# Optimization experiments

Hardware: AMD Instinct MI355X
Metric: run time of the kernel (lower is better)

Reference implementation:

```python
import jax, jax.numpy as jnp
import numpy as np

B, S, E, H = 2, 2048, 512, 8
MLP = 4 * E


def _ln(x, w, b, eps=1e-5):
    m = jnp.mean(x, -1, keepdims=True)
    v = jnp.var(x, -1, keepdims=True)
    return (x - m) / jnp.sqrt(v + eps) * w + b


def setup_inputs() -> dict:
    key = jax.random.key(0)
    ks = jax.random.split(key, 8)
    s = lambda k, shape: (jax.random.normal(k, shape, jnp.float32) * 0.02)
    return {
        "query": jax.random.normal(ks[0], (B, S, E), jnp.float32),
        "attn_gate": jax.random.uniform(ks[1], (B * H, S, S), jnp.float32),
        "in_proj_w": s(ks[2], (3 * E, E)),
        "in_proj_b": jnp.zeros((3 * E,), jnp.float32),
        "out_w": s(ks[3], (E, E)),
        "out_b": jnp.zeros((E,), jnp.float32),
        "ln1_w": jnp.ones((E,), jnp.float32),
        "ln1_b": jnp.zeros((E,), jnp.float32),
        "ln2_w": jnp.ones((E,), jnp.float32),
        "ln2_b": jnp.zeros((E,), jnp.float32),
        "w1": s(ks[4], (MLP, E)),
        "b1": jnp.zeros((MLP,), jnp.float32),
        "w2": s(ks[5], (E, MLP)),
        "b2": jnp.zeros((E,), jnp.float32),
    }


def reference(query, attn_gate, in_proj_w, in_proj_b, out_w, out_b,
              ln1_w, ln1_b, ln2_w, ln2_b, w1, b1, w2, b2):
    b, s, e = query.shape
    h = H
    dh = e // h
    nq = _ln(query, ln1_w, ln1_b)  # pre-LN; key=value=normed query (self-attn)
    Wq, Wk, Wv = jnp.split(in_proj_w, 3, axis=0)
    bq, bk, bv = jnp.split(in_proj_b, 3, axis=0)
    q = nq @ Wq.T + bq
    k = nq @ Wk.T + bk
    v = nq @ Wv.T + bv
    # faithful raw reshape (B,S,E)->(B*H,S,Dh), as in the torch .view
    q = q.reshape(b * h, s, dh)
    k = k.reshape(b * h, s, dh)
    v = v.reshape(b * h, s, dh)
    w = jnp.einsum("bqd,bkd->bqk", q, k)  # no 1/sqrt(d) scaling in source
    w = w * attn_gate
    w = w / (jnp.sum(w, -1, keepdims=True) + 1e-12)  # sum-renormalization
    w = jax.nn.softmax(w, axis=-1)
    o = jnp.einsum("bqk,bkd->bqd", w, v)  # (B*H, S, Dh)
    o = jnp.swapaxes(o, 0, 1).reshape(s, b, e)  # faithful transpose+view
    o = o @ out_w.T + out_b
    o = jnp.swapaxes(o, 0, 1)  # back to batch_first (B,S,E)
    x = query + o
    hmid = _ln(x, ln2_w, ln2_b)
    x = x + (jax.nn.gelu(hmid @ w1.T + b1, approximate=False) @ w2.T + b2)
    attn_weights = w.reshape(b, h, s, s).mean(axis=1)  # average_attn_weights=True
    return (x, attn_weights)
```

## Files before the change

kernel.cpp:

```cpp
#include <hip/hip_runtime.h>
#include <cstdint>
#include <cstddef>

typedef __bf16 bf16_t;
typedef __bf16 bf16x8 __attribute__((ext_vector_type(8)));
typedef float  f32x4  __attribute__((ext_vector_type(4)));

#define S_LEN   2048
#define E_DIM   512
#define H_NUM   8
#define DH      64
#define MLP_DIM 2048

static __device__ __forceinline__ unsigned short f2bfu(float f){
  bf16_t h = (bf16_t)f;
  return __builtin_bit_cast(unsigned short, h);
}

static __device__ __forceinline__ float gelu_f(float v){
  return 0.5f*v*(1.0f + erff(v*0.70710678118654752f));
}

__global__ __launch_bounds__(256) void cvt_kernel(const float* __restrict__ s,
                                                  bf16_t* __restrict__ d, int n){
  int i = (blockIdx.x*256 + threadIdx.x)*4;
  if (i < n){
    float4 v = *(const float4*)(s + i);
    ushort4 pk;
    pk.x = f2bfu(v.x); pk.y = f2bfu(v.y); pk.z = f2bfu(v.z); pk.w = f2bfu(v.w);
    *(ushort4*)((unsigned short*)d + i) = pk;
  }
}

__global__ __launch_bounds__(256) void cvt_split_kernel(const float* __restrict__ s,
                                                        bf16_t* __restrict__ dh,
                                                        bf16_t* __restrict__ dl, int n){
  int i = (blockIdx.x*256 + threadIdx.x)*4;
  if (i < n){
    float4 v = *(const float4*)(s + i);
    float xs[4] = {v.x, v.y, v.z, v.w};
    ushort4 ph, pl;
    unsigned short* hp = (unsigned short*)&ph;
    unsigned short* lp = (unsigned short*)&pl;
    #pragma unroll
    for (int j=0;j<4;j++){
      bf16_t hi = (bf16_t)xs[j];
      bf16_t lo = (bf16_t)(xs[j] - (float)hi);
      hp[j] = __builtin_bit_cast(unsigned short, hi);
      lp[j] = __builtin_bit_cast(unsigned short, lo);
    }
    *(ushort4*)((unsigned short*)dh + i) = ph;
    *(ushort4*)((unsigned short*)dl + i) = pl;
  }
}

__global__ __launch_bounds__(256) void ln_kernel(const float* __restrict__ x,
                                                 const float* __restrict__ w,
                                                 const float* __restrict__ bb,
                                                 bf16_t* __restrict__ out){
  const int row  = blockIdx.x*4 + (threadIdx.x>>6);
  const int lane = threadIdx.x & 63;
  const float* xr = x + (size_t)row*E_DIM + lane*8;
  float4 v0 = *(const float4*)xr;
  float4 v1 = *(const float4*)(xr + 4);
  float xs[8] = {v0.x, v0.y, v0.z, v0.w, v1.x, v1.y, v1.z, v1.w};
  float s = 0.f, s2 = 0.f;
  #pragma unroll
  for (int j=0;j<8;j++){ s += xs[j]; s2 += xs[j]*xs[j]; }
  #pragma unroll
  for (int off=1; off<64; off<<=1){
    s  += __shfl_xor(s,  off, 64);
    s2 += __shfl_xor(s2, off, 64);
  }
  float mean = s*(1.f/512.f);
  float var  = s2*(1.f/512.f) - mean*mean;
  float rstd = rsqrtf(fmaxf(var, 0.f) + 1e-5f);
  const float* wp = w  + lane*8;
  const float* bp = bb + lane*8;
  bf16x8 ov;
  #pragma unroll
  for (int j=0;j<8;j++)
    ov[j] = (bf16_t)((xs[j]-mean)*rstd*wp[j] + bp[j]);
  *(bf16x8*)(out + (size_t)row*E_DIM + lane*8) = ov;
}

__global__ __launch_bounds__(256) void ln_split_kernel(const float* __restrict__ x,
                                                       const float* __restrict__ w,
                                                       const float* __restrict__ bb,
                                                       bf16_t* __restrict__ oh,
                                                       bf16_t* __restrict__ ol){
  const int row  = blockIdx.x*4 + (threadIdx.x>>6);
  const int lane = threadIdx.x & 63;
  const float* xr = x + (size_t)row*E_DIM + lane*8;
  float4 v0 = *(const float4*)xr;
  float4 v1 = *(const float4*)(xr + 4);
  float xs[8] = {v0.x, v0.y, v0.z, v0.w, v1.x, v1.y, v1.z, v1.w};
  float s = 0.f, s2 = 0.f;
  #pragma unroll
  for (int j=0;j<8;j++){ s += xs[j]; s2 += xs[j]*xs[j]; }
  #pragma unroll
  for (int off=1; off<64; off<<=1){
    s  += __shfl_xor(s,  off, 64);
    s2 += __shfl_xor(s2, off, 64);
  }
  float mean = s*(1.f/512.f);
  float var  = s2*(1.f/512.f) - mean*mean;
  float rstd = rsqrtf(fmaxf(var, 0.f) + 1e-5f);
  const float* wp = w  + lane*8;
  const float* bp = bb + lane*8;
  bf16x8 vh, vl;
  #pragma unroll
  for (int j=0;j<8;j++){
    float v = (xs[j]-mean)*rstd*wp[j] + bp[j];
    bf16_t hi = (bf16_t)v;
    vh[j] = hi;
    vl[j] = (bf16_t)(v - (float)hi);
  }
  size_t o = (size_t)row*E_DIM + lane*8;
  *(bf16x8*)(oh + o) = vh;
  *(bf16x8*)(ol + o) = vl;
}

__global__ __launch_bounds__(256) void gemm_qkv_split(
    const bf16_t* __restrict__ Ah, const bf16_t* __restrict__ Al,
    const bf16_t* __restrict__ Bh, const bf16_t* __restrict__ Bl,
    const float* __restrict__ bias,
    bf16_t* __restrict__ qh, bf16_t* __restrict__ ql,
    bf16_t* __restrict__ kh, bf16_t* __restrict__ kl,
    bf16_t* __restrict__ vtmp)
{
  constexpr int TM = 128, TN = 64, BK = 64, MI = 4, NI = 2;
  const int K = 512;

  __shared__ bf16_t Ahs[TM*BK], Als[TM*BK];
  __shared__ bf16_t Bhs[TN*BK], Bls[TN*BK];

  const int tid  = threadIdx.x;
  const int wave = tid>>6, lane = tid&63, quad = lane>>4, l16 = lane&15;
  const int wm = wave>>1, wn = wave&1;

  const int nblk = 1536/TN;
  const int bm = blockIdx.x / nblk;
  const int bn = blockIdx.x % nblk;
  const int m0 = bm*TM, n0 = bn*TN;

  f32x4 acc[MI][NI];
  #pragma unroll
  for (int i=0;i<MI;i++)
    #pragma unroll
    for (int j=0;j<NI;j++)
      acc[i][j] = (f32x4){0.f,0.f,0.f,0.f};

  for (int k0 = 0; k0 < K; k0 += BK){
    bf16x8 avh[4], avl[4], bvh[2], bvl[2];
    #pragma unroll
    for (int i=0;i<4;i++){
      int ga = tid + i*256;
      int row = ga>>3, c8 = (ga&7) ^ (row&7);
      size_t off = (size_t)(m0+row)*K + k0 + c8*8;
      avh[i] = *(const bf16x8*)(Ah + off);
      avl[i] = *(const bf16x8*)(Al + off);
    }
    #pragma unroll
    for (int i=0;i<2;i++){
      int gb = tid + i*256;
      int row = gb>>3, c8 = (gb&7) ^ (row&7);
      size_t off = (size_t)(n0+row)*K + k0 + c8*8;
      bvh[i] = *(const bf16x8*)(Bh + off);
      bvl[i] = *(const bf16x8*)(Bl + off);
    }
    __syncthreads();
    #pragma unroll
    for (int i=0;i<4;i++){
      *(bf16x8*)(Ahs + (size_t)(tid + i*256)*8) = avh[i];
      *(bf16x8*)(Als + (size_t)(tid + i*256)*8) = avl[i];
    }
    #pragma unroll
    for (int i=0;i<2;i++){
      *(bf16x8*)(Bhs + (size_t)(tid + i*256)*8) = bvh[i];
      *(bf16x8*)(Bls + (size_t)(tid + i*256)*8) = bvl[i];
    }
    __syncthreads();
    #pragma unroll
    for (int ks=0;ks<2;ks++){
      bf16x8 afh[MI], afl[MI], bfh[NI], bfl[NI];
      #pragma unroll
      for (int mi=0;mi<MI;mi++){
        int rm = wm*64 + mi*16 + l16;
        size_t sl = (size_t)(rm*8 + ((ks*4+quad) ^ (rm&7)))*8;
        afh[mi] = *(const bf16x8*)(Ahs + sl);
        afl[mi] = *(const bf16x8*)(Als + sl);
      }
      #pragma unroll
      for (int ni=0;ni<NI;ni++){
        int rn = wn*32 + ni*16 + l16;
        size_t sl = (size_t)(rn*8 + ((ks*4+quad) ^ (rn&7)))*8;
        bfh[ni] = *(const bf16x8*)(Bhs + sl);
        bfl[ni] = *(const bf16x8*)(Bls + sl);
      }
      #pragma unroll
      for (int mi=0;mi<MI;mi++)
        #pragma unroll
        for (int ni=0;ni<NI;ni++){
          acc[mi][ni] = __builtin_amdgcn_mfma_f32_16x16x32_bf16(afh[mi], bfh[ni], acc[mi][ni], 0,0,0);
          acc[mi][ni] = __builtin_amdgcn_mfma_f32_16x16x32_bf16(afl[mi], bfh[ni], acc[mi][ni], 0,0,0);
          acc[mi][ni] = __builtin_amdgcn_mfma_f32_16x16x32_bf16(afh[mi], bfl[ni], acc[mi][ni], 0,0,0);
        }
    }
  }

  #pragma unroll
  for (int mi=0;mi<MI;mi++){
    const int grow0 = m0 + wm*64 + mi*16 + quad*4;
    #pragma unroll
    for (int ni=0;ni<NI;ni++){
      const int gcol = n0 + wn*32 + ni*16 + l16;
      const float bvx = bias[gcol];
      if (gcol < 512){
        #pragma unroll
        for (int r=0;r<4;r++){
          float v = acc[mi][ni][r] + bvx;
          size_t idx = (size_t)(grow0+r)*E_DIM + gcol;
          bf16_t hi = (bf16_t)v;
          qh[idx] = hi;
          ql[idx] = (bf16_t)(v - (float)hi);
        }
      } else if (gcol < 1024){
        const int cc = gcol - 512;
        #pragma unroll
        for (int r=0;r<4;r++){
          float v = acc[mi][ni][r] + bvx;
          size_t idx = (size_t)(grow0+r)*E_DIM + cc;
          bf16_t hi = (bf16_t)v;
          kh[idx] = hi;
          kl[idx] = (bf16_t)(v - (float)hi);
        }
      } else {
        const int cc = gcol - 1024;
        #pragma unroll
        for (int r=0;r<4;r++)
          vtmp[(size_t)(grow0+r)*E_DIM + cc] = (bf16_t)(acc[mi][ni][r] + bvx);
      }
    }
  }
}

__global__ __launch_bounds__(256) void vtrans_kernel(const bf16_t* __restrict__ v,
                                                     bf16_t* __restrict__ vt){
  __shared__ bf16_t tile[32*516];
  const int ic = blockIdx.x >> 3;
  const int rg = blockIdx.x & 7;
  const int tid = threadIdx.x;
  const size_t src = ((size_t)ic*256 + rg*32)*E_DIM;
  #pragma unroll
  for (int j=0;j<8;j++){
    int idx = j*2048 + tid*8;
    int row = idx >> 9, col = idx & 511;
    *(bf16x8*)(tile + row*516 + col) = *(const bf16x8*)(v + src + idx);
  }
  __syncthreads();
  #pragma unroll
  for (int j=0;j<8;j++){
    int idx = j*2048 + tid*8;
    int d = idx >> 8;
    int toff = idx & 255;
    int row = toff >> 3;
    bf16x8 o;
    #pragma unroll
    for (int jj=0;jj<8;jj++)
      o[jj] = tile[row*516 + jj*64 + d];
    *(bf16x8*)(vt + ((size_t)ic*64 + d)*S_LEN + rg*256 + toff) = o;
  }
}

template<int TN, int MODE>
__global__ __launch_bounds__(256) void gemm_kernel(
    const bf16_t* __restrict__ A, const bf16_t* __restrict__ Bw,
    const float* __restrict__ bias, int M, int N, int K,
    void* out0, const float* __restrict__ resid)
{
  constexpr int TM = 128;
  constexpr int BK = 64;
  constexpr int MI = 4;
  constexpr int NI = TN/32;
  constexpr int GB = TN/32;

  __shared__ bf16_t As[TM*BK];
  __shared__ bf16_t Bs[TN*BK];

  const int tid  = threadIdx.x;
  const int wave = tid>>6, lane = tid&63, quad = lane>>4, l16 = lane&15;
  const int wm = wave>>1, wn = wave&1;

  const int nblk = N / TN;
  const int bm = blockIdx.x / nblk;
  const int bn = blockIdx.x % nblk;
  const int m0 = bm*TM, n0 = bn*TN;

  f32x4 acc[MI][NI];
  #pragma unroll
  for (int i=0;i<MI;i++)
    #pragma unroll
    for (int j=0;j<NI;j++)
      acc[i][j] = (f32x4){0.f,0.f,0.f,0.f};

  for (int k0 = 0; k0 < K; k0 += BK){
    bf16x8 av[4];
    #pragma unroll
    for (int i=0;i<4;i++){
      int ga = tid + i*256;
      int row = ga>>3, c8 = (ga&7) ^ (row&7);
      av[i] = *(const bf16x8*)(A + (size_t)(m0+row)*K + k0 + c8*8);
    }
    bf16x8 bv[GB];
    #pragma unroll
    for (int i=0;i<GB;i++){
      int gb = tid + i*256;
      int row = gb>>3, c8 = (gb&7) ^ (row&7);
      bv[i] = *(const bf16x8*)(Bw + (size_t)(n0+row)*K + k0 + c8*8);
    }
    __syncthreads();
    #pragma unroll
    for (int i=0;i<4;i++)  *(bf16x8*)(As + (size_t)(tid + i*256)*8) = av[i];
    #pragma unroll
    for (int i=0;i<GB;i++) *(bf16x8*)(Bs + (size_t)(tid + i*256)*8) = bv[i];
    __syncthreads();
    #pragma unroll
    for (int ks=0;ks<2;ks++){
      bf16x8 af[MI], bfr[NI];
      #pragma unroll
      for (int mi=0;mi<MI;mi++){
        int rm = wm*64 + mi*16 + l16;
        af[mi] = *(const bf16x8*)(As + (size_t)(rm*8 + ((ks*4+quad) ^ (rm&7)))*8);
      }
      #pragma unroll
      for (int ni=0;ni<NI;ni++){
        int rn = wn*(TN/2) + ni*16 + l16;
        bfr[ni] = *(const bf16x8*)(Bs + (size_t)(rn*8 + ((ks*4+quad) ^ (rn&7)))*8);
      }
      #pragma unroll
      for (int mi=0;mi<MI;mi++)
        #pragma unroll
        for (int ni=0;ni<NI;ni++)
          acc[mi][ni] = __builtin_amdgcn_mfma_f32_16x16x32_bf16(af[mi], bfr[ni], acc[mi][ni], 0,0,0);
    }
  }

  #pragma unroll
  for (int mi=0;mi<MI;mi++){
    const int grow0 = m0 + wm*64 + mi*16 + quad*4;
    #pragma unroll
    for (int ni=0;ni<NI;ni++){
      const int gcol = n0 + wn*(TN/2) + ni*16 + l16;
      const float bvx = bias[gcol];
      if constexpr (MODE==1){
        float* xo = (float*)out0;
        #pragma unroll
        for (int r=0;r<4;r++){
          size_t idx = (size_t)(grow0+r)*E_DIM + gcol;
          xo[idx] = resid[idx] + acc[mi][ni][r] + bvx;
        }
      } else if constexpr (MODE==2){
        bf16_t* hp = (bf16_t*)out0;
        #pragma unroll
        for (int r=0;r<4;r++)
          hp[(size_t)(grow0+r)*MLP_DIM + gcol] = (bf16_t)gelu_f(acc[mi][ni][r] + bvx);
      } else {
        float* xo = (float*)out0;
        #pragma unroll
        for (int r=0;r<4;r++){
          size_t idx = (size_t)(grow0+r)*E_DIM + gcol;
          xo[idx] = xo[idx] + acc[mi][ni][r] + bvx;
        }
      }
    }
  }
}

__global__ __launch_bounds__(1024) void attn_kernel(
    const bf16_t* __restrict__ qhb, const bf16_t* __restrict__ qlb,
    const bf16_t* __restrict__ khb, const bf16_t* __restrict__ klb,
    const bf16_t* __restrict__ vt,  const float* __restrict__ gate,
    bf16_t* __restrict__ og, float* __restrict__ aw)
{
  __shared__ __align__(16) float u_s[16*2048];
  __shared__ float osh[16*64];
  __shared__ float zsh[16];
  __shared__ float invr_sh[16];
  __shared__ float msh[16];

  const int b   = blockIdx.x >> 7;
  const int sqt = blockIdx.x & 127;
  const int sq0 = sqt*16;

  const int tid = threadIdx.x;
  const int wave = tid>>6, lane = tid&63, quad = lane>>4, l16 = lane&15;

  float awacc[32];
  #pragma unroll
  for (int j=0;j<32;j++) awacc[j] = 0.f;

  f32x4 gpre[8];
  {
    const float* gp = gate + ((size_t)(b*H_NUM)*S_LEN + sq0 + wave)*S_LEN + (size_t)lane*4;
    #pragma unroll
    for (int it=0; it<8; it++)
      gpre[it] = __builtin_nontemporal_load((const f32x4*)(gp + it*256));
  }

  for (int h = 0; h < H_NUM; h++){
    const int bh = b*H_NUM + h;

    osh[tid] = 0.f;
    if (tid < 16) zsh[tid] = 0.f;

    bf16x8 qah0, qah1, qal0, qal1;
    {
      const size_t qoff = ((size_t)bh*S_LEN + sq0 + l16)*DH + quad*8;
      qah0 = *(const bf16x8*)(qhb + qoff);
      qah1 = *(const bf16x8*)(qhb + qoff + 32);
      qal0 = *(const bf16x8*)(qlb + qoff);
      qal1 = *(const bf16x8*)(qlb + qoff + 32);
    }

    for (int cb = wave; cb < 32; cb += 16){
      #pragma unroll
      for (int nb=0; nb<4; nb++){
        const int col0 = cb*64 + nb*16;
        const size_t koff = ((size_t)bh*S_LEN + col0 + l16)*DH + quad*8;
        bf16x8 khf0 = *(const bf16x8*)(khb + koff);
        bf16x8 khf1 = *(const bf16x8*)(khb + koff + 32);
        bf16x8 klf0 = *(const bf16x8*)(klb + koff);
        bf16x8 klf1 = *(const bf16x8*)(klb + koff + 32);
        f32x4 acc = (f32x4){0.f,0.f,0.f,0.f};
        acc = __builtin_amdgcn_mfma_f32_16x16x32_bf16(qah0, khf0, acc, 0,0,0);
        acc = __builtin_amdgcn_mfma_f32_16x16x32_bf16(qah1, khf1, acc, 0,0,0);
        acc = __builtin_amdgcn_mfma_f32_16x16x32_bf16(qal0, khf0, acc, 0,0,0);
        acc = __builtin_amdgcn_mfma_f32_16x16x32_bf16(qal1, khf1, acc, 0,0,0);
        acc = __builtin_amdgcn_mfma_f32_16x16x32_bf16(qah0, klf0, acc, 0,0,0);
        acc = __builtin_amdgcn_mfma_f32_16x16x32_bf16(qah1, klf1, acc, 0,0,0);
        const int c = col0 + l16;
        #pragma unroll
        for (int r=0;r<4;r++){
          const int row = quad*4 + r;
          u_s[row*2048 + (c ^ ((row&7)<<2))] = acc[r];
        }
      }
    }
    __syncthreads();

    {
      f32x4* ub = (f32x4*)u_s + (size_t)wave*512;
      const int sw = wave & 7;
      double s = 0.0;
      float mx = -__builtin_inff(), mn = __builtin_inff();
      #pragma unroll
      for (int it=0; it<8; it++){
        const int c4 = (it*64 + lane) ^ sw;
        f32x4 u = ub[c4];
        u = u * gpre[it];
        ub[c4] = u;
        s += ((double)u[0] + (double)u[1]) + ((double)u[2] + (double)u[3]);
        mx = fmaxf(mx, fmaxf(fmaxf(u[0],u[1]), fmaxf(u[2],u[3])));
        mn = fminf(mn, fminf(fminf(u[0],u[1]), fminf(u[2],u[3])));
      }
      if (h + 1 < H_NUM){
        const float* gp = gate + ((size_t)(b*H_NUM + h + 1)*S_LEN + sq0 + wave)*S_LEN + (size_t)lane*4;
        #pragma unroll
        for (int it=0; it<8; it++)
          gpre[it] = __builtin_nontemporal_load((const f32x4*)(gp + it*256));
      }
      #pragma unroll
      for (int off=1; off<64; off<<=1){
        s  += __shfl_xor(s, off, 64);
        mx = fmaxf(mx, __shfl_xor(mx, off, 64));
        mn = fminf(mn, __shfl_xor(mn, off, 64));
      }
      if (lane == 0){
        double rsum = s + 1e-12;
        float inv = (float)(1.0/rsum);
        invr_sh[wave] = inv;
        msh[wave] = (rsum > 0.0 ? mx : mn) * inv;
      }
    }
    __syncthreads();

    const float inv_r = invr_sh[l16];
    const float m_v   = msh[l16];
    const int nb2 = wave & 3, kh2 = wave >> 2;
    f32x4 oacc = (f32x4){0.f,0.f,0.f,0.f};
    float zp = 0.f;
    const bf16_t* vbase = vt + ((size_t)bh*DH + nb2*16 + l16)*S_LEN;
    const f32x4* ur4 = (const f32x4*)u_s + (size_t)l16*512;
    const int swr = l16 & 7;
    for (int kc = kh2*16; kc < kh2*16 + 16; kc++){
      const int c4a = kc*8 + quad*2;
      f32x4 u0 = ur4[c4a ^ swr];
      f32x4 u1 = ur4[(c4a+1) ^ swr];
      float e0 = __expf(u0[0]*inv_r - m_v);
      float e1 = __expf(u0[1]*inv_r - m_v);
      float e2 = __expf(u0[2]*inv_r - m_v);
      float e3 = __expf(u0[3]*inv_r - m_v);
      float e4 = __expf(u1[0]*inv_r - m_v);
      float e5 = __expf(u1[1]*inv_r - m_v);
      float e6 = __expf(u1[2]*inv_r - m_v);
      float e7 = __expf(u1[3]*inv_r - m_v);
      if (nb2 == 0) zp += ((e0+e1)+(e2+e3)) + ((e4+e5)+(e6+e7));
      bf16x8 pa;
      pa[0]=(bf16_t)e0; pa[1]=(bf16_t)e1; pa[2]=(bf16_t)e2; pa[3]=(bf16_t)e3;
      pa[4]=(bf16_t)e4; pa[5]=(bf16_t)e5; pa[6]=(bf16_t)e6; pa[7]=(bf16_t)e7;
      bf16x8 vf = *(const bf16x8*)(vbase + kc*32 + quad*8);
      oacc = __builtin_amdgcn_mfma_f32_16x16x32_bf16(pa, vf, oacc, 0,0,0);
    }
    if (nb2 == 0){
      zp += __shfl_xor(zp, 16, 64);
      zp += __shfl_xor(zp, 32, 64);
      if (lane < 16) atomicAdd(&zsh[l16], zp);
    }
    #pragma unroll
    for (int r=0;r<4;r++)
      atomicAdd(&osh[(quad*4+r)*64 + nb2*16 + l16], oacc[r]);
    __syncthreads();

    {
      int r = tid >> 6, d = tid & 63;
      float val = osh[tid] / zsh[r];
      og[((size_t)(b*S_LEN + sq0 + r))*E_DIM + h*DH + d] = (bf16_t)val;
    }

    {
      const float inv3 = invr_sh[wave], m3 = msh[wave];
      const float sc = 0.125f / zsh[wave];
      const f32x4* ur3 = (const f32x4*)u_s + (size_t)wave*512;
      const int sw3 = wave & 7;
      #pragma unroll
      for (int g=0; g<8; g++){
        f32x4 u = ur3[(g*64 + lane) ^ sw3];
        awacc[g*4+0] = fmaf(__expf(u[0]*inv3 - m3), sc, awacc[g*4+0]);
        awacc[g*4+1] = fmaf(__expf(u[1]*inv3 - m3), sc, awacc[g*4+1]);
        awacc[g*4+2] = fmaf(__expf(u[2]*inv3 - m3), sc, awacc[g*4+2]);
        awacc[g*4+3] = fmaf(__expf(u[3]*inv3 - m3), sc, awacc[g*4+3]);
      }
    }
    __syncthreads();
  }

  float* awrow = aw + ((size_t)(b*S_LEN) + sq0 + wave)*S_LEN + (size_t)lane*4;
  #pragma unroll
  for (int g=0; g<8; g++){
    f32x4 v = (f32x4){ awacc[g*4+0], awacc[g*4+1], awacc[g*4+2], awacc[g*4+3] };
    __builtin_nontemporal_store(v, (f32x4*)(awrow + g*256));
  }
}

extern "C" void kernel_launch(void* const* d_in, const int* in_sizes, int n_in,
                              void* d_out, int out_size, void* d_ws, size_t ws_size,
                              hipStream_t stream)
{
  const float* query     = (const float*)d_in[0];
  const float* gate      = (const float*)d_in[1];
  const float* in_proj_w = (const float*)d_in[2];
  const float* in_proj_b = (const float*)d_in[3];
  const float* out_w     = (const float*)d_in[4];
  const float* out_b     = (const float*)d_in[5];
  const float* ln1_w     = (const float*)d_in[6];
  const float* ln1_b     = (const float*)d_in[7];
  const float* ln2_w     = (const float*)d_in[8];
  const float* ln2_b     = (const float*)d_in[9];
  const float* w1        = (const float*)d_in[10];
  const float* b1        = (const float*)d_in[11];
  const float* w2        = (const float*)d_in[12];
  const float* b2        = (const float*)d_in[13];

  char* ws = (char*)d_ws;
  bf16_t* nqh   = (bf16_t*)(ws);
  bf16_t* nql   = (bf16_t*)(ws + ((size_t)4<<20));
  bf16_t* qh    = (bf16_t*)(ws + ((size_t)8<<20));
  bf16_t* ql    = (bf16_t*)(ws + ((size_t)12<<20));
  bf16_t* kh    = (bf16_t*)(ws + ((size_t)16<<20));
  bf16_t* kl    = (bf16_t*)(ws + ((size_t)20<<20));
  bf16_t* vtmp  = (bf16_t*)(ws + ((size_t)24<<20));
  bf16_t* vt    = (bf16_t*)(ws + ((size_t)28<<20));
  bf16_t* og    = (bf16_t*)(ws + ((size_t)32<<20));
  bf16_t* hmid  = (bf16_t*)(ws + ((size_t)36<<20));
  bf16_t* h1    = (bf16_t*)(ws + ((size_t)40<<20));
  bf16_t* wqh   = (bf16_t*)(ws + ((size_t)56<<20));
  bf16_t* wql   = (bf16_t*)(ws + ((size_t)58<<20));
  bf16_t* woutb = (bf16_t*)(ws + ((size_t)60<<20));
  bf16_t* w1b   = (bf16_t*)(ws + ((size_t)61<<20));
  bf16_t* w2b   = (bf16_t*)(ws + ((size_t)63<<20));

  float* xout = (float*)d_out;
  float* aw   = xout + (size_t)2*S_LEN*E_DIM;

  cvt_split_kernel<<<768, 256, 0, stream>>>(in_proj_w, wqh, wql, 786432);
  cvt_kernel<<<256, 256, 0, stream>>>(out_w, woutb, 262144);
  cvt_kernel<<<1024,256, 0, stream>>>(w1,    w1b,   1048576);
  cvt_kernel<<<1024,256, 0, stream>>>(w2,    w2b,   1048576);

  ln_split_kernel<<<1024, 256, 0, stream>>>(query, ln1_w, ln1_b, nqh, nql);

  gemm_qkv_split<<<768, 256, 0, stream>>>(nqh, nql, wqh, wql, in_proj_b,
                                          qh, ql, kh, kl, vtmp);

  vtrans_kernel<<<128, 256, 0, stream>>>(vtmp, vt);

  attn_kernel<<<256, 1024, 0, stream>>>(qh, ql, kh, kl, vt, gate, og, aw);

  gemm_kernel<64,1><<<256, 256, 0, stream>>>(og, woutb, out_b,
      4096, 512, 512, (void*)xout, query);

  ln_kernel<<<1024, 256, 0, stream>>>(xout, ln2_w, ln2_b, hmid);

  gemm_kernel<128,2><<<512, 256, 0, stream>>>(hmid, w1b, b1,
      4096, 2048, 512, (void*)h1, nullptr);

  gemm_kernel<64,3><<<256, 256, 0, stream>>>(h1, w2b, b2,
      4096, 512, 2048, (void*)xout, nullptr);
}
```

Baseline: 858.9 us.

## Compute softmax exponentials once into LDS and halve attention block size

The attention kernel now runs 512 threads per block, with each wave handling two query rows. After the row sum and max are found, it computes the exponentials once and writes them back to shared memory. The PV MFMA loop and the head-averaged attention-weight accumulation then read those stored values instead of recomputing exp twice. This removes redundant transcendental work and the zp bookkeeping, and the gate prefetch moves later in the loop. In exchange, each thread holds twice as many accumulator and prefetch registers, and there are half as many waves per block.

```diff
diff --git a/kernel.cpp b/kernel.cpp
--- a/kernel.cpp
+++ b/kernel.cpp
@@ -377,7 +377,8 @@
   }
 }
 
-__global__ __launch_bounds__(1024) void attn_kernel(
+__global__ __launch_bounds__(512) __attribute__((amdgpu_waves_per_eu(2, 2)))
+void attn_kernel(
     const bf16_t* __restrict__ qhb, const bf16_t* __restrict__ qlb,
     const bf16_t* __restrict__ khb, const bf16_t* __restrict__ klb,
     const bf16_t* __restrict__ vt,  const float* __restrict__ gate,
@@ -386,8 +387,6 @@
   __shared__ __align__(16) float u_s[16*2048];
   __shared__ float osh[16*64];
   __shared__ float zsh[16];
-  __shared__ float invr_sh[16];
-  __shared__ float msh[16];
 
   const int b   = blockIdx.x >> 7;
   const int sqt = blockIdx.x & 127;
@@ -396,23 +395,23 @@
   const int tid = threadIdx.x;
   const int wave = tid>>6, lane = tid&63, quad = lane>>4, l16 = lane&15;
 
-  float awacc[32];
-  #pragma unroll
-  for (int j=0;j<32;j++) awacc[j] = 0.f;
-
-  f32x4 gpre[8];
-  {
-    const float* gp = gate + ((size_t)(b*H_NUM)*S_LEN + sq0 + wave)*S_LEN + (size_t)lane*4;
+  float awacc[64];
+  #pragma unroll
+  for (int j=0;j<64;j++) awacc[j] = 0.f;
+
+  f32x4 gpre[2][8];
+  #pragma unroll
+  for (int rr=0;rr<2;rr++){
+    const float* gp = gate + ((size_t)(b*H_NUM)*S_LEN + sq0 + wave*2 + rr)*S_LEN + (size_t)lane*4;
     #pragma unroll
     for (int it=0; it<8; it++)
-      gpre[it] = __builtin_nontemporal_load((const f32x4*)(gp + it*256));
+      gpre[rr][it] = __builtin_nontemporal_load((const f32x4*)(gp + it*256));
   }
 
   for (int h = 0; h < H_NUM; h++){
     const int bh = b*H_NUM + h;
 
-    osh[tid] = 0.f;
-    if (tid < 16) zsh[tid] = 0.f;
+    osh[tid] = 0.f; osh[tid + 512] = 0.f;
 
     bf16x8 qah0, qah1, qal0, qal1;
     {
@@ -423,7 +422,7 @@
       qal1 = *(const bf16x8*)(qlb + qoff + 32);
     }
 
-    for (int cb = wave; cb < 32; cb += 16){
+    for (int cb = wave; cb < 32; cb += 8){
       #pragma unroll
       for (int nb=0; nb<4; nb++){
         const int col0 = cb*64 + nb*16;
@@ -449,26 +448,20 @@
     }
     __syncthreads();
 
-    {
-      f32x4* ub = (f32x4*)u_s + (size_t)wave*512;
-      const int sw = wave & 7;
+    #pragma unroll
+    for (int rr=0; rr<2; rr++){
+      const int row = wave*2 + rr;
+      f32x4* ub = (f32x4*)u_s + (size_t)row*512;
+      const int sw = row & 7;
+      f32x4 uv[8];
       double s = 0.0;
       float mx = -__builtin_inff(), mn = __builtin_inff();
       #pragma unroll
       for (int it=0; it<8; it++){
-        const int c4 = (it*64 + lane) ^ sw;
-        f32x4 u = ub[c4];
-        u = u * gpre[it];
-        ub[c4] = u;
-        s += ((double)u[0] + (double)u[1]) + ((double)u[2] + (double)u[3]);
-        mx = fmaxf(mx, fmaxf(fmaxf(u[0],u[1]), fmaxf(u[2],u[3])));
-        mn = fminf(mn, fminf(fminf(u[0],u[1]), fminf(u[2],u[3])));
-      }
-      if (h + 1 < H_NUM){
-        const float* gp = gate + ((size_t)(b*H_NUM + h + 1)*S_LEN + sq0 + wave)*S_LEN + (size_t)lane*4;
-        #pragma unroll
-        for (int it=0; it<8; it++)
-          gpre[it] = __builtin_nontemporal_load((const f32x4*)(gp + it*256));
+        uv[it] = ub[(it*64 + lane) ^ sw] * gpre[rr][it];
+        s += ((double)uv[it][0] + (double)uv[it][1]) + ((double)uv[it][2] + (double)uv[it][3]);
+        mx = fmaxf(mx, fmaxf(fmaxf(uv[it][0],uv[it][1]), fmaxf(uv[it][2],uv[it][3])));
+        mn = fminf(mn, fminf(fminf(uv[it][0],uv[it][1]), fminf(uv[it][2],uv[it][3])));
       }
       #pragma unroll
       for (int off=1; off<64; off<<=1){
@@ -476,80 +469,93 @@
         mx = fmaxf(mx, __shfl_xor(mx, off, 64));
         mn = fminf(mn, __shfl_xor(mn, off, 64));
       }
-      if (lane == 0){
-        double rsum = s + 1e-12;
-        float inv = (float)(1.0/rsum);
-        invr_sh[wave] = inv;
-        msh[wave] = (rsum > 0.0 ? mx : mn) * inv;
-      }
-    }
-    __syncthreads();
-
-    const float inv_r = invr_sh[l16];
-    const float m_v   = msh[l16];
-    const int nb2 = wave & 3, kh2 = wave >> 2;
-    f32x4 oacc = (f32x4){0.f,0.f,0.f,0.f};
-    float zp = 0.f;
-    const bf16_t* vbase = vt + ((size_t)bh*DH + nb2*16 + l16)*S_LEN;
-    const f32x4* ur4 = (const f32x4*)u_s + (size_t)l16*512;
-    const int swr = l16 & 7;
-    for (int kc = kh2*16; kc < kh2*16 + 16; kc++){
-      const int c4a = kc*8 + quad*2;
-      f32x4 u0 = ur4[c4a ^ swr];
-      f32x4 u1 = ur4[(c4a+1) ^ swr];
-      float e0 = __expf(u0[0]*inv_r - m_v);
-      float e1 = __expf(u0[1]*inv_r - m_v);
-      float e2 = __expf(u0[2]*inv_r - m_v);
-      float e3 = __expf(u0[3]*inv_r - m_v);
-      float e4 = __expf(u1[0]*inv_r - m_v);
-      float e5 = __expf(u1[1]*inv_r - m_v);
-      float e6 = __expf(u1[2]*inv_r - m_v);
-      float e7 = __expf(u1[3]*inv_r - m_v);
-      if (nb2 == 0) zp += ((e0+e1)+(e2+e3)) + ((e4+e5)+(e6+e7));
-      bf16x8 pa;
-      pa[0]=(bf16_t)e0; pa[1]=(bf16_t)e1; pa[2]=(bf16_t)e2; pa[3]=(bf16_t)e3;
-      pa[4]=(bf16_t)e4; pa[5]=(bf16_t)e5; pa[6]=(bf16_t)e6; pa[7]=(bf16_t)e7;
-      bf16x8 vf = *(const bf16x8*)(vbase + kc*32 + quad*8);
-      oacc = __builtin_amdgcn_mfma_f32_16x16x32_bf16(pa, vf, oacc, 0,0,0);
-    }
-    if (nb2 == 0){
-      zp += __shfl_xor(zp, 16, 64);
-      zp += __shfl_xor(zp, 32, 64);
-      if (lane < 16) atomicAdd(&zsh[l16], zp);
-    }
-    #pragma unroll
-    for (int r=0;r<4;r++)
-      atomicAdd(&osh[(quad*4+r)*64 + nb2*16 + l16], oacc[r]);
+      const double rsum = s + 1e-12;
+      const float inv = (float)(1.0/rsum);
+      const float m = (rsum > 0.0 ? mx : mn) * inv;
+      float z = 0.f;
+      #pragma unroll
+      for (int it=0; it<8; it++){
+        f32x4 e;
+        e[0] = __expf(uv[it][0]*inv - m);
+        e[1] = __expf(uv[it][1]*inv - m);
+        e[2] = __expf(uv[it][2]*inv - m);
+        e[3] = __expf(uv[it][3]*inv - m);
+        ub[(it*64 + lane) ^ sw] = e;
+        z += (e[0]+e[1]) + (e[2]+e[3]);
+      }
+      #pragma unroll
+      for (int off=1; off<64; off<<=1) z += __shfl_xor(z, off, 64);
+      if (lane == 0) zsh[row] = z;
+    }
     __syncthreads();
 
     {
-      int r = tid >> 6, d = tid & 63;
-      float val = osh[tid] / zsh[r];
+      const int nb2 = wave & 3, khh = wave >> 2;
+      f32x4 oacc = (f32x4){0.f,0.f,0.f,0.f};
+      const bf16_t* vbase = vt + ((size_t)bh*DH + nb2*16 + l16)*S_LEN;
+      const f32x4* ur4 = (const f32x4*)u_s + (size_t)l16*512;
+      const int swr = l16 & 7;
+      #pragma unroll 4
+      for (int kc = khh*32; kc < khh*32 + 32; kc++){
+        const int c4a = kc*8 + quad*2;
+        f32x4 e0 = ur4[c4a ^ swr];
+        f32x4 e1 = ur4[(c4a+1) ^ swr];
+        bf16x8 pa;
+        pa[0]=(bf16_t)e0[0]; pa[1]=(bf16_t)e0[1]; pa[2]=(bf16_t)e0[2]; pa[3]=(bf16_t)e0[3];
+        pa[4]=(bf16_t)e1[0]; pa[5]=(bf16_t)e1[1]; pa[6]=(bf16_t)e1[2]; pa[7]=(bf16_t)e1[3];
+        bf16x8 vf = *(const bf16x8*)(vbase + kc*32 + quad*8);
+        oacc = __builtin_amdgcn_mfma_f32_16x16x32_bf16(pa, vf, oacc, 0,0,0);
+      }
+      #pragma unroll
+      for (int r=0;r<4;r++)
+        atomicAdd(&osh[(quad*4+r)*64 + nb2*16 + l16], oacc[r]);
+    }
+    __syncthreads();
+
+    #pragma unroll
+    for (int t = tid; t < 1024; t += 512){
+      int r = t >> 6, d = t & 63;
+      float val = osh[t] / zsh[r];
       og[((size_t)(b*S_LEN + sq0 + r))*E_DIM + h*DH + d] = (bf16_t)val;
     }
 
-    {
-      const float inv3 = invr_sh[wave], m3 = msh[wave];
-      const float sc = 0.125f / zsh[wave];
-      const f32x4* ur3 = (const f32x4*)u_s + (size_t)wave*512;
-      const int sw3 = wave & 7;
+    if (h + 1 < H_NUM){
+      #pragma unroll
+      for (int rr=0;rr<2;rr++){
+        const float* gp = gate + ((size_t)(b*H_NUM + h + 1)*S_LEN + sq0 + wave*2 + rr)*S_LEN + (size_t)lane*4;
+        #pragma unroll
+        for (int it=0; it<8; it++)
+          gpre[rr][it] = __builtin_nontemporal_load((const f32x4*)(gp + it*256));
+      }
+    }
+
+    #pragma unroll
+    for (int rr=0; rr<2; rr++){
+      const int row = wave*2 + rr;
+      const float sc = 0.125f / zsh[row];
+      const f32x4* ur3 = (const f32x4*)u_s + (size_t)row*512;
+      const int sw3 = row & 7;
       #pragma unroll
       for (int g=0; g<8; g++){
-        f32x4 u = ur3[(g*64 + lane) ^ sw3];
-        awacc[g*4+0] = fmaf(__expf(u[0]*inv3 - m3), sc, awacc[g*4+0]);
-        awacc[g*4+1] = fmaf(__expf(u[1]*inv3 - m3), sc, awacc[g*4+1]);
-        awacc[g*4+2] = fmaf(__expf(u[2]*inv3 - m3), sc, awacc[g*4+2]);
-        awacc[g*4+3] = fmaf(__expf(u[3]*inv3 - m3), sc, awacc[g*4+3]);
-      }
-    }
-    __syncthreads();
-  }
-
-  float* awrow = aw + ((size_t)(b*S_LEN) + sq0 + wave)*S_LEN + (size_t)lane*4;
-  #pragma unroll
-  for (int g=0; g<8; g++){
-    f32x4 v = (f32x4){ awacc[g*4+0], awacc[g*4+1], awacc[g*4+2], awacc[g*4+3] };
-    __builtin_nontemporal_store(v, (f32x4*)(awrow + g*256));
+        f32x4 e = ur3[(g*64 + lane) ^ sw3];
+        awacc[rr*32+g*4+0] = fmaf(e[0], sc, awacc[rr*32+g*4+0]);
+        awacc[rr*32+g*4+1] = fmaf(e[1], sc, awacc[rr*32+g*4+1]);
+        awacc[rr*32+g*4+2] = fmaf(e[2], sc, awacc[rr*32+g*4+2]);
+        awacc[rr*32+g*4+3] = fmaf(e[3], sc, awacc[rr*32+g*4+3]);
+      }
+    }
+    __syncthreads();
+  }
+
+  #pragma unroll
+  for (int rr=0; rr<2; rr++){
+    float* awrow = aw + ((size_t)(b*S_LEN) + sq0 + wave*2 + rr)*S_LEN + (size_t)lane*4;
+    #pragma unroll
+    for (int g=0; g<8; g++){
+      f32x4 v = (f32x4){ awacc[rr*32+g*4+0], awacc[rr*32+g*4+1],
+                         awacc[rr*32+g*4+2], awacc[rr*32+g*4+3] };
+      __builtin_nontemporal_store(v, (f32x4*)(awrow + g*256));
+    }
   }
 }
 
@@ -605,7 +611,7 @@
 
   vtrans_kernel<<<128, 256, 0, stream>>>(vtmp, vt);
 
-  attn_kernel<<<256, 1024, 0, stream>>>(qh, ql, kh, kl, vt, gate, og, aw);
+  attn_kernel<<<256, 512, 0, stream>>>(qh, ql, kh, kl, vt, gate, og, aw);
 
   gemm_kernel<64,1><<<256, 256, 0, stream>>>(og, woutb, out_b,
       4096, 512, 512, (void*)xout, query);
```

New measurement: 705.8 us. -17.8%, faster.
